# Kernel optimization log

Measured on AMD Instinct MI355X. Metric: run time of the kernel, lower is better.

Reference implementation:

```python
import jax, jax.numpy as jnp
import numpy as np

CUTOFF = 5.0   # cutoff radius (init kwarg)
EPS = 1e-7     # wrap_positions eps
MIN_DIST = 0.01


def _wrap_positions(pos, cell):
    # pos: [N,3], cell: [3,3] (rows are lattice vectors)
    scaled = pos @ jnp.linalg.inv(cell) + EPS
    scaled = scaled % 1.0 - EPS
    return scaled @ cell


def setup_inputs() -> dict:
    key = jax.random.key(0)
    B, N, L = 4, 512, 30.0  # 4 systems, 512 atoms each, ~30A cubic cells
    k1, k2 = jax.random.split(key)
    positions = jax.random.uniform(k1, (B * N, 3), dtype=jnp.float32) * L
    # near-cubic cells with a small perturbation (invertible, edge >> cutoff)
    cell = jnp.eye(3, dtype=jnp.float32)[None, :, :] * L \
        + 0.1 * jax.random.normal(k2, (B, 3, 3), dtype=jnp.float32)
    n_atoms = jnp.full((B,), N, dtype=jnp.int32)
    return {"positions": positions, "cell": cell, "n_atoms": n_atoms}


def reference(positions, cell, n_atoms):
    # positions: [B*N,3] flat batch, cell: [B,3,3], n_atoms: [B] (all equal N)
    B = cell.shape[0]
    N = positions.shape[0] // B
    pos = positions.reshape(B, N, 3)

    r = jnp.arange(-1, 2)
    # 27 periodic image shifts, same as disp_mat / padding_mat with padding=1
    shifts = jnp.stack(jnp.meshgrid(r, r, r, indexing='ij'), axis=-1)
    shifts = shifts.reshape(-1, 3).astype(positions.dtype)  # [27,3]

    def one_system(p, c):
        wp = _wrap_positions(p, c)          # [N,3]
        sc = shifts @ c                      # [27,3] cartesian shift vectors
        # diff[i,j,s] = (wp[j] + shift_s) - wp[i]  -> pair_diff of torch code
        diff = wp[None, :, None, :] + sc[None, None, :, :] - wp[:, None, None, :]  # [N,N,27,3]
        dist = jnp.linalg.norm(diff, axis=-1)                                       # [N,N,27]
        mask = (dist < CUTOFF) & (dist > MIN_DIST)
        return diff * mask[..., None], dist * mask, mask

    # dense masked equivalent of the compacted (pairs, pair_diff, pair_dist)
    return jax.vmap(one_system)(pos, cell)
```

## Files before the change

### kernel.cpp

```cpp
#include <hip/hip_runtime.h>
#include <math.h>

#define CUTOFF_F 5.0f
#define MIN_DIST_F 0.01f
#define EPS_D 1e-7

__global__ void bnl_prep(const float* __restrict__ pos,
                         const float* __restrict__ cell,
                         float* __restrict__ wp,
                         float* __restrict__ sc,
                         int B, int N) {
    int tid = blockIdx.x * blockDim.x + threadIdx.x;
    int nthreads = gridDim.x * blockDim.x;

    for (int t = tid; t < B * 27; t += nthreads) {
        int b = t / 27, s = t - b * 27;
        int sx = s / 9 - 1;
        int sy = (s / 3) % 3 - 1;
        int sz = s - (s / 3) * 3 - 1;
        const float* c = cell + b * 9;
        sc[t * 3 + 0] = (float)((double)sx * c[0] + (double)sy * c[3] + (double)sz * c[6]);
        sc[t * 3 + 1] = (float)((double)sx * c[1] + (double)sy * c[4] + (double)sz * c[7]);
        sc[t * 3 + 2] = (float)((double)sx * c[2] + (double)sy * c[5] + (double)sz * c[8]);
    }

    int total = B * N;
    for (int n = tid; n < total; n += nthreads) {
        int b = n / N;
        const float* c = cell + b * 9;
        double a00 = c[0], a01 = c[1], a02 = c[2];
        double a10 = c[3], a11 = c[4], a12 = c[5];
        double a20 = c[6], a21 = c[7], a22 = c[8];
        double co00 =  (a11 * a22 - a12 * a21);
        double co01 = -(a10 * a22 - a12 * a20);
        double co02 =  (a10 * a21 - a11 * a20);
        double det = a00 * co00 + a01 * co01 + a02 * co02;
        double id = 1.0 / det;
        double m00 = co00 * id;
        double m01 = -(a01 * a22 - a02 * a21) * id;
        double m02 =  (a01 * a12 - a02 * a11) * id;
        double m10 = co01 * id;
        double m11 =  (a00 * a22 - a02 * a20) * id;
        double m12 = -(a00 * a12 - a02 * a10) * id;
        double m20 = co02 * id;
        double m21 = -(a00 * a21 - a01 * a20) * id;
        double m22 =  (a00 * a11 - a01 * a10) * id;

        double p0 = pos[n * 3 + 0], p1 = pos[n * 3 + 1], p2 = pos[n * 3 + 2];
        double s0 = p0 * m00 + p1 * m10 + p2 * m20 + EPS_D;
        double s1 = p0 * m01 + p1 * m11 + p2 * m21 + EPS_D;
        double s2 = p0 * m02 + p1 * m12 + p2 * m22 + EPS_D;
        s0 -= floor(s0); s1 -= floor(s1); s2 -= floor(s2);
        s0 -= EPS_D; s1 -= EPS_D; s2 -= EPS_D;
        wp[n * 3 + 0] = (float)(s0 * a00 + s1 * a10 + s2 * a20);
        wp[n * 3 + 1] = (float)(s0 * a01 + s1 * a11 + s2 * a21);
        wp[n * 3 + 2] = (float)(s0 * a02 + s1 * a12 + s2 * a22);
    }
}

__global__ __launch_bounds__(256) void bnl_fill2(const float* __restrict__ wp,
                                                 const float* __restrict__ sc,
                                                 float* __restrict__ out,
                                                 int B, int N) {
    extern __shared__ float lds[];
    float* lwp = lds;
    float* lsc = lds + N * 3;

    int b = blockIdx.x / N;
    int i = blockIdx.x - b * N;

    const float* wrow = wp + (size_t)b * N * 3;
    int nf4 = (N * 3) >> 2;
    for (int t = threadIdx.x; t < nf4; t += blockDim.x)
        reinterpret_cast<float4*>(lwp)[t] = reinterpret_cast<const float4*>(wrow)[t];
    for (int t = (nf4 << 2) + threadIdx.x; t < N * 3; t += blockDim.x)
        lwp[t] = wrow[t];
    for (int t = threadIdx.x; t < 81; t += blockDim.x)
        lsc[t] = sc[(size_t)b * 81 + t];
    __syncthreads();

    float pix = lwp[i * 3 + 0];
    float piy = lwp[i * 3 + 1];
    float piz = lwp[i * 3 + 2];

    size_t D1  = (size_t)B * N * N * 27;
    size_t row = (size_t)(b * N + i) * N * 27;
    float* diff_out = out + row * 3;
    float* dist_out = out + 3 * D1 + row;
    float* mask_out = out + 4 * D1 + row;

    int NP = N * 27;
    int NQ = NP >> 2;

    for (int q = threadIdx.x; q < NQ; q += blockDim.x) {
        float dv[12], tv[4], mv[4];
        int p0 = q << 2;
#pragma unroll
        for (int k = 0; k < 4; ++k) {
            unsigned p = (unsigned)(p0 + k);
            unsigned j = p / 27u;
            unsigned s = p - j * 27u;
            float dx = lwp[j * 3 + 0] + lsc[s * 3 + 0] - pix;
            float dy = lwp[j * 3 + 1] + lsc[s * 3 + 1] - piy;
            float dz = lwp[j * 3 + 2] + lsc[s * 3 + 2] - piz;
            float dist = sqrtf(dx * dx + dy * dy + dz * dz);
            bool m = (dist < CUTOFF_F) && (dist > MIN_DIST_F);
            dv[k * 3 + 0] = m ? dx : 0.0f;
            dv[k * 3 + 1] = m ? dy : 0.0f;
            dv[k * 3 + 2] = m ? dz : 0.0f;
            tv[k] = m ? dist : 0.0f;
            mv[k] = m ? 1.0f : 0.0f;
        }
        float4* dp = reinterpret_cast<float4*>(diff_out + (size_t)p0 * 3);
        dp[0] = make_float4(dv[0], dv[1], dv[2],  dv[3]);
        dp[1] = make_float4(dv[4], dv[5], dv[6],  dv[7]);
        dp[2] = make_float4(dv[8], dv[9], dv[10], dv[11]);
        *reinterpret_cast<float4*>(dist_out + p0) = make_float4(tv[0], tv[1], tv[2], tv[3]);
        *reinterpret_cast<float4*>(mask_out + p0) = make_float4(mv[0], mv[1], mv[2], mv[3]);
    }
}

extern "C" void kernel_launch(void* const* d_in, const int* in_sizes, int n_in,
                              void* d_out, int out_size, void* d_ws, size_t ws_size,
                              hipStream_t stream) {
    const float* pos  = (const float*)d_in[0];
    const float* cell = (const float*)d_in[1];
    int B = in_sizes[1] / 9;
    int N = in_sizes[0] / (3 * B);

    float* wp = (float*)d_ws;
    float* sc = wp + (size_t)B * N * 3;

    bnl_prep<<<8, 256, 0, stream>>>(pos, cell, wp, sc, B, N);

    size_t lds_bytes = ((size_t)N * 3 + 81) * sizeof(float);
    bnl_fill2<<<B * N, 256, lds_bytes, stream>>>(wp, sc, (float*)d_out, B, N);
}
```

Baseline: 114.4 us.

## Use nontemporal stores, split rows across two blocks, incrementalize pair indexing

Output stores switch to nontemporal vector stores to stream the large masked output past the caches. Each row of i is split across two blocks that each cover half of j, doubling the grid and halving LDS per block. The per-element divide by 27 is replaced with an incremental counter, and the prep kernel gets more blocks. The kernel is mostly write-bandwidth bound, so compute savings may matter little.

Result: slower. 353.6 us (+209.2%).

```diff
diff --git a/kernel.cpp b/kernel.cpp
--- a/kernel.cpp
+++ b/kernel.cpp
@@ -4,6 +4,13 @@
 #define CUTOFF_F 5.0f
 #define MIN_DIST_F 0.01f
 #define EPS_D 1e-7
+
+typedef float f32x4 __attribute__((ext_vector_type(4)));
+
+static __device__ __forceinline__ void nt_store4(float* p, float a, float b, float c, float d) {
+    f32x4 v = {a, b, c, d};
+    __builtin_nontemporal_store(v, reinterpret_cast<f32x4*>(p));
+}
 
 __global__ void bnl_prep(const float* __restrict__ pos,
                          const float* __restrict__ cell,
@@ -58,48 +65,51 @@
     }
 }
 
-__global__ __launch_bounds__(256) void bnl_fill2(const float* __restrict__ wp,
+__global__ __launch_bounds__(256) void bnl_fill3(const float* __restrict__ wp,
                                                  const float* __restrict__ sc,
                                                  float* __restrict__ out,
                                                  int B, int N) {
     extern __shared__ float lds[];
+    const int Nh = N >> 1;
     float* lwp = lds;
-    float* lsc = lds + N * 3;
+    float* lsc = lds + Nh * 3;
 
-    int b = blockIdx.x / N;
-    int i = blockIdx.x - b * N;
+    int blk  = blockIdx.x;
+    int b    = blk / (N * 2);
+    int rem  = blk - b * (N * 2);
+    int i    = rem >> 1;
+    int half = rem & 1;
+    int jbase = half * Nh;
 
-    const float* wrow = wp + (size_t)b * N * 3;
-    int nf4 = (N * 3) >> 2;
+    const float* wrow = wp + ((size_t)b * N + jbase) * 3;
+    int nf4 = (Nh * 3) >> 2;
     for (int t = threadIdx.x; t < nf4; t += blockDim.x)
-        reinterpret_cast<float4*>(lwp)[t] = reinterpret_cast<const float4*>(wrow)[t];
-    for (int t = (nf4 << 2) + threadIdx.x; t < N * 3; t += blockDim.x)
+        reinterpret_cast<f32x4*>(lwp)[t] = reinterpret_cast<const f32x4*>(wrow)[t];
+    for (int t = (nf4 << 2) + threadIdx.x; t < Nh * 3; t += blockDim.x)
         lwp[t] = wrow[t];
     for (int t = threadIdx.x; t < 81; t += blockDim.x)
         lsc[t] = sc[(size_t)b * 81 + t];
     __syncthreads();
 
-    float pix = lwp[i * 3 + 0];
-    float piy = lwp[i * 3 + 1];
-    float piz = lwp[i * 3 + 2];
+    const float* pip = wp + ((size_t)b * N + i) * 3;
+    float pix = pip[0], piy = pip[1], piz = pip[2];
 
-    size_t D1  = (size_t)B * N * N * 27;
-    size_t row = (size_t)(b * N + i) * N * 27;
-    float* diff_out = out + row * 3;
-    float* dist_out = out + 3 * D1 + row;
-    float* mask_out = out + 4 * D1 + row;
+    size_t D1   = (size_t)B * N * N * 27;
+    size_t NPh  = (size_t)Nh * 27;
+    size_t base = (size_t)(b * N + i) * N * 27 + (size_t)half * NPh;
+    float* diff_out = out + base * 3;
+    float* dist_out = out + 3 * D1 + base;
+    float* mask_out = out + 4 * D1 + base;
 
-    int NP = N * 27;
-    int NQ = NP >> 2;
+    int NQ = (int)(NPh >> 2);
 
     for (int q = threadIdx.x; q < NQ; q += blockDim.x) {
         float dv[12], tv[4], mv[4];
         int p0 = q << 2;
+        unsigned j = (unsigned)p0 / 27u;
+        unsigned s = (unsigned)p0 - j * 27u;
 #pragma unroll
         for (int k = 0; k < 4; ++k) {
-            unsigned p = (unsigned)(p0 + k);
-            unsigned j = p / 27u;
-            unsigned s = p - j * 27u;
             float dx = lwp[j * 3 + 0] + lsc[s * 3 + 0] - pix;
             float dy = lwp[j * 3 + 1] + lsc[s * 3 + 1] - piy;
             float dz = lwp[j * 3 + 2] + lsc[s * 3 + 2] - piz;
@@ -110,13 +120,15 @@
             dv[k * 3 + 2] = m ? dz : 0.0f;
             tv[k] = m ? dist : 0.0f;
             mv[k] = m ? 1.0f : 0.0f;
+            ++s;
+            if (s == 27u) { s = 0u; ++j; }
         }
-        float4* dp = reinterpret_cast<float4*>(diff_out + (size_t)p0 * 3);
-        dp[0] = make_float4(dv[0], dv[1], dv[2],  dv[3]);
-        dp[1] = make_float4(dv[4], dv[5], dv[6],  dv[7]);
-        dp[2] = make_float4(dv[8], dv[9], dv[10], dv[11]);
-        *reinterpret_cast<float4*>(dist_out + p0) = make_float4(tv[0], tv[1], tv[2], tv[3]);
-        *reinterpret_cast<float4*>(mask_out + p0) = make_float4(mv[0], mv[1], mv[2], mv[3]);
+        float* dp = diff_out + (size_t)p0 * 3;
+        nt_store4(dp + 0, dv[0], dv[1], dv[2],  dv[3]);
+        nt_store4(dp + 4, dv[4], dv[5], dv[6],  dv[7]);
+        nt_store4(dp + 8, dv[8], dv[9], dv[10], dv[11]);
+        nt_store4(dist_out + p0, tv[0], tv[1], tv[2], tv[3]);
+        nt_store4(mask_out + p0, mv[0], mv[1], mv[2], mv[3]);
     }
 }
 
@@ -131,8 +143,8 @@
     float* wp = (float*)d_ws;
     float* sc = wp + (size_t)B * N * 3;
 
-    bnl_prep<<<8, 256, 0, stream>>>(pos, cell, wp, sc, B, N);
+    bnl_prep<<<32, 256, 0, stream>>>(pos, cell, wp, sc, B, N);
 
-    size_t lds_bytes = ((size_t)N * 3 + 81) * sizeof(float);
-    bnl_fill2<<<B * N, 256, lds_bytes, stream>>>(wp, sc, (float*)d_out, B, N);
+    size_t lds_bytes = ((size_t)(N / 2) * 3 + 81) * sizeof(float);
+    bnl_fill3<<<B * N * 2, 256, lds_bytes, stream>>>(wp, sc, (float*)d_out, B, N);
 }
```

## Remap workgroups across XCDs, unroll two quads per thread, incremental index math

Applied to the files above, without the earlier changes.

Workgroup IDs are remapped so that consecutive output rows land on the same XCD (an 8-way chunked swizzle). The fill loop now handles two quads per thread per iteration to raise store-level parallelism. The per-element divide by 27 is replaced with one divide per quad plus incremental index updates. The prep kernel grid is also enlarged. The kernel is bound by writing roughly 100M+ floats of output, so these tweaks mainly target store throughput and L2 locality, at the cost of more registers per thread.

Measured after the change: 124.3 us. +8.7%, slower.

```diff
diff --git a/kernel.cpp b/kernel.cpp
--- a/kernel.cpp
+++ b/kernel.cpp
@@ -4,6 +4,8 @@
 #define CUTOFF_F 5.0f
 #define MIN_DIST_F 0.01f
 #define EPS_D 1e-7
+
+typedef float f32x4 __attribute__((ext_vector_type(4)));
 
 __global__ void bnl_prep(const float* __restrict__ pos,
                          const float* __restrict__ cell,
@@ -58,7 +60,7 @@
     }
 }
 
-__global__ __launch_bounds__(256) void bnl_fill2(const float* __restrict__ wp,
+__global__ __launch_bounds__(256) void bnl_fill5(const float* __restrict__ wp,
                                                  const float* __restrict__ sc,
                                                  float* __restrict__ out,
                                                  int B, int N) {
@@ -66,13 +68,19 @@
     float* lwp = lds;
     float* lsc = lds + N * 3;
 
-    int b = blockIdx.x / N;
-    int i = blockIdx.x - b * N;
+    int nwg = gridDim.x;
+    int blk = blockIdx.x;
+    if ((nwg & 7) == 0) {
+        int chunk = nwg >> 3;
+        blk = (blk & 7) * chunk + (blk >> 3);
+    }
+    int b = blk / N;
+    int i = blk - b * N;
 
     const float* wrow = wp + (size_t)b * N * 3;
     int nf4 = (N * 3) >> 2;
     for (int t = threadIdx.x; t < nf4; t += blockDim.x)
-        reinterpret_cast<float4*>(lwp)[t] = reinterpret_cast<const float4*>(wrow)[t];
+        reinterpret_cast<f32x4*>(lwp)[t] = reinterpret_cast<const f32x4*>(wrow)[t];
     for (int t = (nf4 << 2) + threadIdx.x; t < N * 3; t += blockDim.x)
         lwp[t] = wrow[t];
     for (int t = threadIdx.x; t < 81; t += blockDim.x)
@@ -89,34 +97,73 @@
     float* dist_out = out + 3 * D1 + row;
     float* mask_out = out + 4 * D1 + row;
 
-    int NP = N * 27;
-    int NQ = NP >> 2;
+    int NQ = (N * 27) >> 2;
+    int BD = blockDim.x;
 
-    for (int q = threadIdx.x; q < NQ; q += blockDim.x) {
-        float dv[12], tv[4], mv[4];
-        int p0 = q << 2;
+    for (int q0 = 0; q0 < NQ; q0 += 2 * BD) {
+        float dvA[12], tvA[4], mvA[4];
+        float dvB[12], tvB[4], mvB[4];
+        int qA = q0 + threadIdx.x;
+        int qB = qA + BD;
+        bool hasA = qA < NQ;
+        bool hasB = qB < NQ;
+
+        if (hasA) {
+            int p0 = qA << 2;
+            unsigned j = (unsigned)p0 / 27u;
+            unsigned s = (unsigned)p0 - j * 27u;
 #pragma unroll
-        for (int k = 0; k < 4; ++k) {
-            unsigned p = (unsigned)(p0 + k);
-            unsigned j = p / 27u;
-            unsigned s = p - j * 27u;
-            float dx = lwp[j * 3 + 0] + lsc[s * 3 + 0] - pix;
-            float dy = lwp[j * 3 + 1] + lsc[s * 3 + 1] - piy;
-            float dz = lwp[j * 3 + 2] + lsc[s * 3 + 2] - piz;
-            float dist = sqrtf(dx * dx + dy * dy + dz * dz);
-            bool m = (dist < CUTOFF_F) && (dist > MIN_DIST_F);
-            dv[k * 3 + 0] = m ? dx : 0.0f;
-            dv[k * 3 + 1] = m ? dy : 0.0f;
-            dv[k * 3 + 2] = m ? dz : 0.0f;
-            tv[k] = m ? dist : 0.0f;
-            mv[k] = m ? 1.0f : 0.0f;
+            for (int k = 0; k < 4; ++k) {
+                float dx = lwp[j * 3 + 0] + lsc[s * 3 + 0] - pix;
+                float dy = lwp[j * 3 + 1] + lsc[s * 3 + 1] - piy;
+                float dz = lwp[j * 3 + 2] + lsc[s * 3 + 2] - piz;
+                float dist = sqrtf(dx * dx + dy * dy + dz * dz);
+                bool m = (dist < CUTOFF_F) && (dist > MIN_DIST_F);
+                dvA[k * 3 + 0] = m ? dx : 0.0f;
+                dvA[k * 3 + 1] = m ? dy : 0.0f;
+                dvA[k * 3 + 2] = m ? dz : 0.0f;
+                tvA[k] = m ? dist : 0.0f;
+                mvA[k] = m ? 1.0f : 0.0f;
+                ++s;
+                if (s == 27u) { s = 0u; ++j; }
+            }
         }
-        float4* dp = reinterpret_cast<float4*>(diff_out + (size_t)p0 * 3);
-        dp[0] = make_float4(dv[0], dv[1], dv[2],  dv[3]);
-        dp[1] = make_float4(dv[4], dv[5], dv[6],  dv[7]);
-        dp[2] = make_float4(dv[8], dv[9], dv[10], dv[11]);
-        *reinterpret_cast<float4*>(dist_out + p0) = make_float4(tv[0], tv[1], tv[2], tv[3]);
-        *reinterpret_cast<float4*>(mask_out + p0) = make_float4(mv[0], mv[1], mv[2], mv[3]);
+        if (hasB) {
+            int p0 = qB << 2;
+            unsigned j = (unsigned)p0 / 27u;
+            unsigned s = (unsigned)p0 - j * 27u;
+#pragma unroll
+            for (int k = 0; k < 4; ++k) {
+                float dx = lwp[j * 3 + 0] + lsc[s * 3 + 0] - pix;
+                float dy = lwp[j * 3 + 1] + lsc[s * 3 + 1] - piy;
+                float dz = lwp[j * 3 + 2] + lsc[s * 3 + 2] - piz;
+                float dist = sqrtf(dx * dx + dy * dy + dz * dz);
+                bool m = (dist < CUTOFF_F) && (dist > MIN_DIST_F);
+                dvB[k * 3 + 0] = m ? dx : 0.0f;
+                dvB[k * 3 + 1] = m ? dy : 0.0f;
+                dvB[k * 3 + 2] = m ? dz : 0.0f;
+                tvB[k] = m ? dist : 0.0f;
+                mvB[k] = m ? 1.0f : 0.0f;
+                ++s;
+                if (s == 27u) { s = 0u; ++j; }
+            }
+        }
+        if (hasA) {
+            f32x4* dp = reinterpret_cast<f32x4*>(diff_out + (size_t)(qA << 2) * 3);
+            dp[0] = (f32x4){dvA[0], dvA[1], dvA[2],  dvA[3]};
+            dp[1] = (f32x4){dvA[4], dvA[5], dvA[6],  dvA[7]};
+            dp[2] = (f32x4){dvA[8], dvA[9], dvA[10], dvA[11]};
+            *reinterpret_cast<f32x4*>(dist_out + ((size_t)qA << 2)) = (f32x4){tvA[0], tvA[1], tvA[2], tvA[3]};
+            *reinterpret_cast<f32x4*>(mask_out + ((size_t)qA << 2)) = (f32x4){mvA[0], mvA[1], mvA[2], mvA[3]};
+        }
+        if (hasB) {
+            f32x4* dp = reinterpret_cast<f32x4*>(diff_out + (size_t)(qB << 2) * 3);
+            dp[0] = (f32x4){dvB[0], dvB[1], dvB[2],  dvB[3]};
+            dp[1] = (f32x4){dvB[4], dvB[5], dvB[6],  dvB[7]};
+            dp[2] = (f32x4){dvB[8], dvB[9], dvB[10], dvB[11]};
+            *reinterpret_cast<f32x4*>(dist_out + ((size_t)qB << 2)) = (f32x4){tvB[0], tvB[1], tvB[2], tvB[3]};
+            *reinterpret_cast<f32x4*>(mask_out + ((size_t)qB << 2)) = (f32x4){mvB[0], mvB[1], mvB[2], mvB[3]};
+        }
     }
 }
 
@@ -131,8 +178,8 @@
     float* wp = (float*)d_ws;
     float* sc = wp + (size_t)B * N * 3;
 
-    bnl_prep<<<8, 256, 0, stream>>>(pos, cell, wp, sc, B, N);
+    bnl_prep<<<32, 256, 0, stream>>>(pos, cell, wp, sc, B, N);
 
     size_t lds_bytes = ((size_t)N * 3 + 81) * sizeof(float);
-    bnl_fill2<<<B * N, 256, lds_bytes, stream>>>(wp, sc, (float*)d_out, B, N);
+    bnl_fill5<<<B * N, 256, lds_bytes, stream>>>(wp, sc, (float*)d_out, B, N);
 }
```

## Fuse position wrapping into the fill kernel and drop per-element div-by-27

Applied to the files above, without the earlier changes.

Removes the separate prep kernel: each block recomputes the cell inverse, the wrapped positions for its whole system and the 27 shift vectors directly into LDS, then fills its output row. This saves a kernel launch, the workspace round trip and the dependency between kernels. In exchange every block redoes O(N) double-precision wrapping work (2048 blocks each wrapping 512 atoms). The inner loop also computes j/s with one division per quad and increments them, instead of dividing for every element.

New measurement: 126.6 us. +10.7%, slower.

```diff
diff --git a/kernel.cpp b/kernel.cpp
--- a/kernel.cpp
+++ b/kernel.cpp
@@ -5,32 +5,24 @@
 #define MIN_DIST_F 0.01f
 #define EPS_D 1e-7
 
-__global__ void bnl_prep(const float* __restrict__ pos,
-                         const float* __restrict__ cell,
-                         float* __restrict__ wp,
-                         float* __restrict__ sc,
-                         int B, int N) {
-    int tid = blockIdx.x * blockDim.x + threadIdx.x;
-    int nthreads = gridDim.x * blockDim.x;
+typedef float f32x4 __attribute__((ext_vector_type(4)));
 
-    for (int t = tid; t < B * 27; t += nthreads) {
-        int b = t / 27, s = t - b * 27;
-        int sx = s / 9 - 1;
-        int sy = (s / 3) % 3 - 1;
-        int sz = s - (s / 3) * 3 - 1;
-        const float* c = cell + b * 9;
-        sc[t * 3 + 0] = (float)((double)sx * c[0] + (double)sy * c[3] + (double)sz * c[6]);
-        sc[t * 3 + 1] = (float)((double)sx * c[1] + (double)sy * c[4] + (double)sz * c[7]);
-        sc[t * 3 + 2] = (float)((double)sx * c[2] + (double)sy * c[5] + (double)sz * c[8]);
-    }
+__global__ __launch_bounds__(256) void bnl_fused(const float* __restrict__ pos,
+                                                 const float* __restrict__ cell,
+                                                 float* __restrict__ out,
+                                                 int B, int N) {
+    extern __shared__ float lds[];
+    float* lwp = lds;
+    float* lsc = lds + N * 3;
 
-    int total = B * N;
-    for (int n = tid; n < total; n += nthreads) {
-        int b = n / N;
-        const float* c = cell + b * 9;
-        double a00 = c[0], a01 = c[1], a02 = c[2];
-        double a10 = c[3], a11 = c[4], a12 = c[5];
-        double a20 = c[6], a21 = c[7], a22 = c[8];
+    int b = blockIdx.x / N;
+    int i = blockIdx.x - b * N;
+
+    const float* c = cell + b * 9;
+    double a00 = c[0], a01 = c[1], a02 = c[2];
+    double a10 = c[3], a11 = c[4], a12 = c[5];
+    double a20 = c[6], a21 = c[7], a22 = c[8];
+    {
         double co00 =  (a11 * a22 - a12 * a21);
         double co01 = -(a10 * a22 - a12 * a20);
         double co02 =  (a10 * a21 - a11 * a20);
@@ -46,37 +38,30 @@
         double m21 = -(a00 * a21 - a01 * a20) * id;
         double m22 =  (a00 * a11 - a01 * a10) * id;
 
-        double p0 = pos[n * 3 + 0], p1 = pos[n * 3 + 1], p2 = pos[n * 3 + 2];
-        double s0 = p0 * m00 + p1 * m10 + p2 * m20 + EPS_D;
-        double s1 = p0 * m01 + p1 * m11 + p2 * m21 + EPS_D;
-        double s2 = p0 * m02 + p1 * m12 + p2 * m22 + EPS_D;
-        s0 -= floor(s0); s1 -= floor(s1); s2 -= floor(s2);
-        s0 -= EPS_D; s1 -= EPS_D; s2 -= EPS_D;
-        wp[n * 3 + 0] = (float)(s0 * a00 + s1 * a10 + s2 * a20);
-        wp[n * 3 + 1] = (float)(s0 * a01 + s1 * a11 + s2 * a21);
-        wp[n * 3 + 2] = (float)(s0 * a02 + s1 * a12 + s2 * a22);
+        for (int n = threadIdx.x; n < N; n += blockDim.x) {
+            const float* p = pos + ((size_t)b * N + n) * 3;
+            double p0 = p[0], p1 = p[1], p2 = p[2];
+            double s0 = p0 * m00 + p1 * m10 + p2 * m20 + EPS_D;
+            double s1 = p0 * m01 + p1 * m11 + p2 * m21 + EPS_D;
+            double s2 = p0 * m02 + p1 * m12 + p2 * m22 + EPS_D;
+            s0 -= floor(s0); s1 -= floor(s1); s2 -= floor(s2);
+            s0 -= EPS_D; s1 -= EPS_D; s2 -= EPS_D;
+            lwp[n * 3 + 0] = (float)(s0 * a00 + s1 * a10 + s2 * a20);
+            lwp[n * 3 + 1] = (float)(s0 * a01 + s1 * a11 + s2 * a21);
+            lwp[n * 3 + 2] = (float)(s0 * a02 + s1 * a12 + s2 * a22);
+        }
+        if (threadIdx.x < 81) {
+            int s  = threadIdx.x / 3;
+            int cc = threadIdx.x - s * 3;
+            double sx = (double)(s / 9 - 1);
+            double sy = (double)((s / 3) % 3 - 1);
+            double sz = (double)(s % 3 - 1);
+            double col0 = (cc == 0) ? a00 : (cc == 1) ? a01 : a02;
+            double col1 = (cc == 0) ? a10 : (cc == 1) ? a11 : a12;
+            double col2 = (cc == 0) ? a20 : (cc == 1) ? a21 : a22;
+            lsc[threadIdx.x] = (float)(sx * col0 + sy * col1 + sz * col2);
+        }
     }
-}
-
-__global__ __launch_bounds__(256) void bnl_fill2(const float* __restrict__ wp,
-                                                 const float* __restrict__ sc,
-                                                 float* __restrict__ out,
-                                                 int B, int N) {
-    extern __shared__ float lds[];
-    float* lwp = lds;
-    float* lsc = lds + N * 3;
-
-    int b = blockIdx.x / N;
-    int i = blockIdx.x - b * N;
-
-    const float* wrow = wp + (size_t)b * N * 3;
-    int nf4 = (N * 3) >> 2;
-    for (int t = threadIdx.x; t < nf4; t += blockDim.x)
-        reinterpret_cast<float4*>(lwp)[t] = reinterpret_cast<const float4*>(wrow)[t];
-    for (int t = (nf4 << 2) + threadIdx.x; t < N * 3; t += blockDim.x)
-        lwp[t] = wrow[t];
-    for (int t = threadIdx.x; t < 81; t += blockDim.x)
-        lsc[t] = sc[(size_t)b * 81 + t];
     __syncthreads();
 
     float pix = lwp[i * 3 + 0];
@@ -89,17 +74,15 @@
     float* dist_out = out + 3 * D1 + row;
     float* mask_out = out + 4 * D1 + row;
 
-    int NP = N * 27;
-    int NQ = NP >> 2;
+    int NQ = (N * 27) >> 2;
 
     for (int q = threadIdx.x; q < NQ; q += blockDim.x) {
         float dv[12], tv[4], mv[4];
         int p0 = q << 2;
+        unsigned j = (unsigned)p0 / 27u;
+        unsigned s = (unsigned)p0 - j * 27u;
 #pragma unroll
         for (int k = 0; k < 4; ++k) {
-            unsigned p = (unsigned)(p0 + k);
-            unsigned j = p / 27u;
-            unsigned s = p - j * 27u;
             float dx = lwp[j * 3 + 0] + lsc[s * 3 + 0] - pix;
             float dy = lwp[j * 3 + 1] + lsc[s * 3 + 1] - piy;
             float dz = lwp[j * 3 + 2] + lsc[s * 3 + 2] - piz;
@@ -110,13 +93,15 @@
             dv[k * 3 + 2] = m ? dz : 0.0f;
             tv[k] = m ? dist : 0.0f;
             mv[k] = m ? 1.0f : 0.0f;
+            ++s;
+            if (s == 27u) { s = 0u; ++j; }
         }
-        float4* dp = reinterpret_cast<float4*>(diff_out + (size_t)p0 * 3);
-        dp[0] = make_float4(dv[0], dv[1], dv[2],  dv[3]);
-        dp[1] = make_float4(dv[4], dv[5], dv[6],  dv[7]);
-        dp[2] = make_float4(dv[8], dv[9], dv[10], dv[11]);
-        *reinterpret_cast<float4*>(dist_out + p0) = make_float4(tv[0], tv[1], tv[2], tv[3]);
-        *reinterpret_cast<float4*>(mask_out + p0) = make_float4(mv[0], mv[1], mv[2], mv[3]);
+        f32x4* dp = reinterpret_cast<f32x4*>(diff_out + (size_t)p0 * 3);
+        dp[0] = (f32x4){dv[0], dv[1], dv[2],  dv[3]};
+        dp[1] = (f32x4){dv[4], dv[5], dv[6],  dv[7]};
+        dp[2] = (f32x4){dv[8], dv[9], dv[10], dv[11]};
+        *reinterpret_cast<f32x4*>(dist_out + (size_t)p0) = (f32x4){tv[0], tv[1], tv[2], tv[3]};
+        *reinterpret_cast<f32x4*>(mask_out + (size_t)p0) = (f32x4){mv[0], mv[1], mv[2], mv[3]};
     }
 }
 
@@ -128,11 +113,6 @@
     int B = in_sizes[1] / 9;
     int N = in_sizes[0] / (3 * B);
 
-    float* wp = (float*)d_ws;
-    float* sc = wp + (size_t)B * N * 3;
-
-    bnl_prep<<<8, 256, 0, stream>>>(pos, cell, wp, sc, B, N);
-
     size_t lds_bytes = ((size_t)N * 3 + 81) * sizeof(float);
-    bnl_fill2<<<B * N, 256, lds_bytes, stream>>>(wp, sc, (float*)d_out, B, N);
+    bnl_fused<<<B * N, 256, lds_bytes, stream>>>(pos, cell, (float*)d_out, B, N);
 }
```
